# Kernel optimization log

Hardware: AMD Instinct MI355X
Metric: run time of the kernel (lower is better)

Reference implementation:

```python
import jax, jax.numpy as jnp
import numpy as np

N = 100000
E = 1600000
IN_C, HID_C, OUT_C = 128, 128, 10
NUM_GRAPHS = 64


def gcn_conv(x, src, dst, dinv, W, b, n_nodes):
    # x: [N, Fin]; src/dst: [E+N] (self-loops included); dinv: [N]
    xw = x @ W                                   # [N, Fout]
    norm = dinv[src] * dinv[dst]                 # [E+N]
    msg = xw[src] * norm[:, None]                # [E+N, Fout]
    return jax.ops.segment_sum(msg, dst, num_segments=n_nodes) + b


def setup_inputs() -> dict:
    key = jax.random.key(0)
    k1, k2, k3, k4, k5, k6, k7, k8 = jax.random.split(key, 8)
    x = jax.random.normal(k1, (N, IN_C), dtype=jnp.float32)
    edge_index = jax.random.randint(k2, (2, E), 0, N, dtype=jnp.int64)
    batch = jnp.sort(jax.random.randint(k3, (N,), 0, NUM_GRAPHS, dtype=jnp.int64))
    s1 = 1.0 / np.sqrt(IN_C)
    s2 = 1.0 / np.sqrt(HID_C)
    W1 = jax.random.uniform(k4, (IN_C, HID_C), jnp.float32, -s1, s1)
    b1 = jnp.zeros((HID_C,), jnp.float32)
    W2 = jax.random.uniform(k5, (HID_C, HID_C), jnp.float32, -s2, s2)
    b2 = jnp.zeros((HID_C,), jnp.float32)
    Wlin = jax.random.uniform(k6, (HID_C, OUT_C), jnp.float32, -s2, s2)
    blin = jax.random.uniform(k7, (OUT_C,), jnp.float32, -s2, s2)
    return {"x": x, "edge_index": edge_index, "batch": batch,
            "W1": W1, "b1": b1, "W2": W2, "b2": b2,
            "Wlin": Wlin, "blin": blin}


def reference(x, edge_index, batch, W1, b1, W2, b2, Wlin, blin):
    n = x.shape[0]
    loop = jnp.arange(n, dtype=edge_index.dtype)
    src = jnp.concatenate([edge_index[0], loop])   # self-loops appended
    dst = jnp.concatenate([edge_index[1], loop])
    deg = jax.ops.segment_sum(jnp.ones_like(dst, dtype=x.dtype), dst, num_segments=n)
    dinv = jnp.where(deg > 0, jax.lax.rsqrt(deg), 0.0)

    h = jax.nn.relu(gcn_conv(x, src, dst, dinv, W1, b1, n))
    h = jax.nn.relu(gcn_conv(h, src, dst, dinv, W2, b2, n))

    # global mean pool over graphs
    sums = jax.ops.segment_sum(h, batch, num_segments=NUM_GRAPHS)          # [G, H]
    cnts = jax.ops.segment_sum(jnp.ones((n,), h.dtype), batch, num_segments=NUM_GRAPHS)
    pooled = sums / jnp.maximum(cnts, 1.0)[:, None]
    return pooled @ Wlin + blin                                            # [G, OUT_C]
```

## Files before the change

### kernel.cpp

```cpp
#include <hip/hip_runtime.h>


#define TPB 256
#define R_LOG 7
#define R_NODES 128
#define NB_MAX 800
#define CH 8192
#define CAP_LOG 12
#define CAP 4096

#define FS 16.0f
#define FSI (1.0f / 16.0f)

typedef __attribute__((ext_vector_type(8))) short short8;
typedef __attribute__((ext_vector_type(4))) float f32x4;
typedef __attribute__((ext_vector_type(2))) float f32x2;

__device__ inline ushort f2bf(float x) {
    uint u = __float_as_uint(x);
    return (ushort)((u + 0x7FFFu + ((u >> 16) & 1u)) >> 16);
}

__global__ __launch_bounds__(1024) void bin_pass(const int* __restrict__ src,
                                                 const int* __restrict__ dst, int e,
                                                 int* __restrict__ gbcur,
                                                 int* __restrict__ buck, int nb) {
    __shared__ int vloc[CH];
    __shared__ ushort bidl[CH];
    __shared__ int cnts[NB_MAX], starts[NB_MAX], cnts2[NB_MAX];
    int t = threadIdx.x;
    for (int i = t; i < nb; i += 1024) { cnts[i] = 0; cnts2[i] = 0; }
    __syncthreads();
    int base = blockIdx.x * CH;
    int lim = base + CH; if (lim > e) lim = e;
    int ce = lim - base;
    int nv = ce >> 2;
    const int4* s4 = (const int4*)(src + base);
    const int4* d4 = (const int4*)(dst + base);
    for (int i = t; i < nv; i += 1024) {
        int4 s = s4[i], d = d4[i];
        int j = i << 2;
#define BIN1(J, SS, DD)                                                      \
        { int b_ = (DD) >> R_LOG;                                            \
          vloc[J] = ((SS) << R_LOG) | ((DD) & (R_NODES - 1));                \
          bidl[J] = (ushort)b_;                                              \
          atomicAdd(&cnts[b_], 1); }
        BIN1(j,     s.x, d.x)
        BIN1(j + 1, s.y, d.y)
        BIN1(j + 2, s.z, d.z)
        BIN1(j + 3, s.w, d.w)
    }
    for (int j = (nv << 2) + t; j < ce; j += 1024) {
        int dv = dst[base + j], sv = src[base + j];
        BIN1(j, sv, dv)
    }
#undef BIN1
    __syncthreads();
    for (int i = t; i < nb; i += 1024) {
        int c = cnts[i];
        starts[i] = c ? ((i << CAP_LOG) + atomicAdd(&gbcur[i], c)) : 0;
    }
    __syncthreads();
    for (int j = t; j < ce; j += 1024) {
        int b = bidl[j];
        int pos = starts[b] + atomicAdd(&cnts2[b], 1);
        if (pos < ((b + 1) << CAP_LOG))
            buck[pos] = vloc[j];
    }
}

__global__ __launch_bounds__(256) void count_pass(const int* __restrict__ buck,
                                                  const int* __restrict__ gbcur,
                                                  int* __restrict__ cnt,
                                                  float* __restrict__ dinv,
                                                  int* __restrict__ bktsum,
                                                  uint* __restrict__ t1z,
                                                  uint* __restrict__ t2z, int n) {
    __shared__ int c128[R_NODES];
    __shared__ int wred[4];
    int t = threadIdx.x;
    int b = blockIdx.x;
    if (b == 0 && t < 32) { t1z[t] = 0; t2z[t] = 0; }
    if (t < R_NODES) c128[t] = 0;
    __syncthreads();
    int beg = b << CAP_LOG;
    int fill = gbcur[b]; if (fill > CAP) fill = CAP;
    int end = beg + fill;
    int nv = fill >> 2;
    const int4* b4 = (const int4*)(buck + beg);
    for (int i = t; i < nv; i += 256) {
        int4 v = b4[i];
        atomicAdd(&c128[v.x & (R_NODES - 1)], 1);
        atomicAdd(&c128[v.y & (R_NODES - 1)], 1);
        atomicAdd(&c128[v.z & (R_NODES - 1)], 1);
        atomicAdd(&c128[v.w & (R_NODES - 1)], 1);
    }
    for (int i = beg + (nv << 2) + t; i < end; i += 256)
        atomicAdd(&c128[buck[i] & (R_NODES - 1)], 1);
    __syncthreads();
    int node = (b << R_LOG) + t;
    int pv = 0;
    if (t < R_NODES && node < n) {
        int c = c128[t];
        cnt[node] = c;
        dinv[node] = rsqrtf((float)(c + 1));
        pv = (c + 7) & ~7;
    }
    for (int o = 32; o; o >>= 1) pv += __shfl_down(pv, o);
    int lane = t & 63, wid = t >> 6;
    if (lane == 0) wred[wid] = pv;
    __syncthreads();
    if (t == 0) bktsum[b] = wred[0] + wred[1] + wred[2] + wred[3];
}

__device__ __forceinline__ void csr_body(int b, const int* __restrict__ buck,
                                         const int* __restrict__ cnt,
                                         const int* __restrict__ bktsum,
                                         const int* __restrict__ gbcur,
                                         int n, int nbkt, int* __restrict__ ew,
                                         int* __restrict__ rowptr) {
    __shared__ int rbase[R_NODES];
    __shared__ int cur[R_NODES];
    __shared__ int wtot[8], sred[8];
    int t = threadIdx.x;
    int n0 = b << R_LOG;
    int n1 = n0 + R_NODES; if (n1 > n) n1 = n;
    int nn = n1 - n0;
    int lane = t & 63, wid = t >> 6;
    int s = 0;
    for (int i = t; i < b; i += 512) s += bktsum[i];
    for (int o = 32; o; o >>= 1) s += __shfl_down(s, o);
    if (lane == 0) sred[wid] = s;
    int v = (t < nn) ? ((cnt[n0 + t] + 7) & ~7) : 0;
    int x = v;
    for (int o = 1; o < 64; o <<= 1) {
        int y = __shfl_up(x, o);
        if (lane >= o) x += y;
    }
    if (lane == 63) wtot[wid] = x;
    __syncthreads();
    int base = sred[0] + sred[1] + sred[2] + sred[3] +
               sred[4] + sred[5] + sred[6] + sred[7];
    int add = (wid == 1) ? wtot[0] : 0;
    int excl = base + x - v + add;
    if (t < nn) {
        rbase[t] = excl;
        rowptr[n0 + t] = excl;
        cur[t] = 0;
    }
    int endoff = base + wtot[0] + wtot[1];
    if (b == nbkt - 1 && t == 0) rowptr[n] = endoff;
    __syncthreads();
    int beg = b << CAP_LOG;
    int fill = gbcur[b]; if (fill > CAP) fill = CAP;
    int end = beg + fill;
    int nv = fill >> 2;
    const int4* bb4 = (const int4*)(buck + beg);
#define SCAT(VV) { int ld_ = (VV) & (R_NODES - 1);                       \
                   int p_ = rbase[ld_] + atomicAdd(&cur[ld_], 1);        \
                   ew[p_] = (VV) >> R_LOG; }
    for (int i = t; i < nv; i += 512) {
        int4 vv = bb4[i];
        SCAT(vv.x) SCAT(vv.y) SCAT(vv.z) SCAT(vv.w)
    }
    for (int i = beg + (nv << 2) + t; i < end; i += 512) {
        int vv = buck[i];
        SCAT(vv)
    }
#undef SCAT
    __syncthreads();
    if (t < nn) {
        int pe = (t + 1 < nn) ? rbase[t + 1] : endoff;
        for (int j = rbase[t] + cur[t]; j < pe; ++j) ew[j] = n;
    }
}

__device__ __forceinline__ void gemm1_body(int blk, const float* __restrict__ Av,
                                           const float* __restrict__ W,
                                           const float* __restrict__ dinv,
                                           uchar* __restrict__ C, int n) {
    __shared__ ushort Wt[128 * 136];
    int t = threadIdx.x;
    for (int idx = t; idx < 128 * 128; idx += 512) {
        int k = idx >> 7, nn = idx & 127;
        Wt[nn * 136 + k] = f2bf(W[idx]);
    }
    __syncthreads();

    int w = t >> 6, l = t & 63;
    int r0 = blk * 256;
    int lrow = l & 15, lhk = (l >> 4) * 8;

    short8 afrag[2][4];
    for (int mt = 0; mt < 2; ++mt) {
        int row = r0 + mt * 128 + w * 16 + lrow;
        bool ok = row < n;
        for (int ks = 0; ks < 4; ++ks) {
            int kb = ks * 32 + lhk;
            short8 f = {0, 0, 0, 0, 0, 0, 0, 0};
            if (ok) {
                const float* ap = Av + (size_t)row * 128 + kb;
                float4 u0 = *(const float4*)ap;
                float4 u1 = *(const float4*)(ap + 4);
                f[0] = (short)f2bf(u0.x); f[1] = (short)f2bf(u0.y);
                f[2] = (short)f2bf(u0.z); f[3] = (short)f2bf(u0.w);
                f[4] = (short)f2bf(u1.x); f[5] = (short)f2bf(u1.y);
                f[6] = (short)f2bf(u1.z); f[7] = (short)f2bf(u1.w);
            }
            afrag[mt][ks] = f;
        }
    }

    f32x4 acc[2][8];
    for (int mt = 0; mt < 2; ++mt)
        for (int nt = 0; nt < 8; ++nt)
            acc[mt][nt] = (f32x4){0.f, 0.f, 0.f, 0.f};

#pragma unroll
    for (int ks = 0; ks < 4; ++ks)
#pragma unroll
        for (int nt = 0; nt < 8; ++nt) {
            short8 b = *(const short8*)&Wt[(nt * 16 + lrow) * 136 + ks * 32 + lhk];
            acc[0][nt] = __builtin_amdgcn_mfma_f32_16x16x32_bf16(afrag[0][ks], b, acc[0][nt], 0, 0, 0);
            acc[1][nt] = __builtin_amdgcn_mfma_f32_16x16x32_bf16(afrag[1][ks], b, acc[1][nt], 0, 0, 0);
        }

    __syncthreads();
    uchar* Cs = (uchar*)Wt;
    int rb = (l >> 4) * 4;
    for (int mt = 0; mt < 2; ++mt)
        for (int r = 0; r < 4; ++r) {
            int lr = mt * 128 + w * 16 + rb + r;
            int rr = r0 + lr;
            float di = (rr < n) ? dinv[rr] * FS : 0.f;
            for (int nt = 0; nt < 8; ++nt) {
                float v = acc[mt][nt][r] * di;
                uint bb = (uint)__builtin_amdgcn_cvt_pk_fp8_f32(v, v, 0, false);
                Cs[lr * 128 + nt * 16 + lrow] = (uchar)(bb & 0xFF);
            }
        }
    __syncthreads();
    for (int idx = t; idx < 2048; idx += 512) {
        int rr = idx >> 3, cc = (idx & 7) * 16;
        int row2 = r0 + rr;
        if (row2 < n)
            *(uint4*)(C + (size_t)row2 * 128 + cc) = *(const uint4*)&Cs[rr * 128 + cc];
    }
}

__global__ __launch_bounds__(512) void csr_gemm1(const int* __restrict__ buck,
                                                 const int* __restrict__ cnt,
                                                 const int* __restrict__ bktsum,
                                                 const int* __restrict__ gbcur,
                                                 int n, int nbkt,
                                                 int* __restrict__ ew,
                                                 int* __restrict__ rowptr,
                                                 const float* __restrict__ x,
                                                 const float* __restrict__ W1,
                                                 const float* __restrict__ dinv,
                                                 uchar* __restrict__ T1) {
    int b = blockIdx.x;
    if (b < nbkt)
        csr_body(b, buck, cnt, bktsum, gbcur, n, nbkt, ew, rowptr);
    else
        gemm1_body(b - nbkt, x, W1, dinv, T1, n);
}

__global__ __launch_bounds__(512) void gemm2_pool(const ushort* __restrict__ A,
                                                  const float* __restrict__ W,
                                                  const float* __restrict__ bias,
                                                  const int* __restrict__ batch,
                                                  float* __restrict__ gsum,
                                                  float* __restrict__ gcnt, int n) {
    __shared__ ushort Wt[128 * 136];
    __shared__ float pg[2][128];
    __shared__ int bloc[256];
    __shared__ int cnt01[2];
    __shared__ int g01[2];
    int t = threadIdx.x;
    int r0 = blockIdx.x * 256;
    for (int idx = t; idx < 128 * 128; idx += 512) {
        int k = idx >> 7, nn = idx & 127;
        Wt[nn * 136 + k] = f2bf(W[idx]);
    }
    if (t < 256) {
        int row = r0 + t;
        bloc[t] = (row < n) ? batch[row] : -1;
    }
    if (t < 128) { pg[0][t] = 0.f; pg[1][t] = 0.f; }
    if (t < 2) cnt01[t] = 0;
    __syncthreads();
    if (t == 0) {
        g01[0] = bloc[0];
        int j = 255; while (j > 0 && bloc[j] < 0) --j;
        g01[1] = bloc[j];
    }

    int w = t >> 6, l = t & 63;
    int lrow = l & 15, lhk = (l >> 4) * 8;

    short8 afrag[2][4];
    for (int mt = 0; mt < 2; ++mt) {
        int row = r0 + mt * 128 + w * 16 + lrow;
        bool ok = row < n;
        for (int ks = 0; ks < 4; ++ks) {
            short8 f = {0, 0, 0, 0, 0, 0, 0, 0};
            if (ok) f = *(const short8*)(A + (size_t)row * 128 + ks * 32 + lhk);
            afrag[mt][ks] = f;
        }
    }

    f32x4 acc[2][8];
    for (int mt = 0; mt < 2; ++mt)
        for (int nt = 0; nt < 8; ++nt)
            acc[mt][nt] = (f32x4){0.f, 0.f, 0.f, 0.f};

#pragma unroll
    for (int ks = 0; ks < 4; ++ks)
#pragma unroll
        for (int nt = 0; nt < 8; ++nt) {
            short8 b = *(const short8*)&Wt[(nt * 16 + lrow) * 136 + ks * 32 + lhk];
            acc[0][nt] = __builtin_amdgcn_mfma_f32_16x16x32_bf16(afrag[0][ks], b, acc[0][nt], 0, 0, 0);
            acc[1][nt] = __builtin_amdgcn_mfma_f32_16x16x32_bf16(afrag[1][ks], b, acc[1][nt], 0, 0, 0);
        }
    __syncthreads();

    int g0 = g01[0], g1 = g01[1];
    float bch[8];
#pragma unroll
    for (int nt = 0; nt < 8; ++nt) bch[nt] = bias[nt * 16 + lrow];
    float ch0[8], ch1[8];
#pragma unroll
    for (int nt = 0; nt < 8; ++nt) { ch0[nt] = 0.f; ch1[nt] = 0.f; }
    int rb = (l >> 4) * 4;
    int c0 = 0, c1 = 0;
    for (int mt = 0; mt < 2; ++mt)
        for (int r = 0; r < 4; ++r) {
            int lr = mt * 128 + w * 16 + rb + r;
            int rr = r0 + lr;
            if (rr >= n) continue;
            int g = bloc[lr];
            if (g == g0) {
#pragma unroll
                for (int nt = 0; nt < 8; ++nt)
                    ch0[nt] += fmaxf(acc[mt][nt][r] + bch[nt], 0.f);
                if (lrow == 0) c0++;
            } else if (g == g1) {
#pragma unroll
                for (int nt = 0; nt < 8; ++nt)
                    ch1[nt] += fmaxf(acc[mt][nt][r] + bch[nt], 0.f);
                if (lrow == 0) c1++;
            } else {
#pragma unroll
                for (int nt = 0; nt < 8; ++nt)
                    atomicAdd(&gsum[g * 128 + nt * 16 + lrow],
                              fmaxf(acc[mt][nt][r] + bch[nt], 0.f));
                if (lrow == 0) atomicAdd(&gcnt[g], 1.f);
            }
        }
#pragma unroll
    for (int nt = 0; nt < 8; ++nt) {
        int ch = nt * 16 + lrow;
        atomicAdd(&pg[0][ch], ch0[nt]);
        atomicAdd(&pg[1][ch], ch1[nt]);
    }
    if (lrow == 0) {
        if (c0) atomicAdd(&cnt01[0], c0);
        if (c1) atomicAdd(&cnt01[1], c1);
    }
    __syncthreads();
    if (t < 128) {
        atomicAdd(&gsum[g0 * 128 + t], pg[0][t]);
        if (g1 != g0) atomicAdd(&gsum[g1 * 128 + t], pg[1][t]);
    }
    if (t == 0) {
        atomicAdd(&gcnt[g0], (float)cnt01[0]);
        if (g1 != g0) atomicAdd(&gcnt[g1], (float)cnt01[1]);
    }
}

#define LDG2(s) (*(const uint2*)(xwb + ((((uint)(s)) << 7) + clo)))
#define ACCU(G)                                                             \
    { f32x2 p01 = __builtin_amdgcn_cvt_pk_f32_fp8((int)(G).x, false);       \
      f32x2 p23 = __builtin_amdgcn_cvt_pk_f32_fp8((int)(G).x, true);        \
      f32x2 p45 = __builtin_amdgcn_cvt_pk_f32_fp8((int)(G).y, false);       \
      f32x2 p67 = __builtin_amdgcn_cvt_pk_f32_fp8((int)(G).y, true);        \
      a0 += p01.x; a1 += p01.y; a2 += p23.x; a3 += p23.y;                   \
      a4 += p45.x; a5 += p45.y; a6 += p67.x; a7 += p67.y; }

template <int MODE>
__global__ __launch_bounds__(256) void agg_gather(const uchar* __restrict__ tab,
                                                  const int* __restrict__ ewsrc,
                                                  const int* __restrict__ rowptr,
                                                  const float* __restrict__ dinv,
                                                  const float* __restrict__ bias,
                                                  void* __restrict__ outp, int n) {
    int node = blockIdx.x * 4 + (threadIdx.x >> 6);
    if (node >= n) return;
    int lane = threadIdx.x & 63;
    int q = lane >> 4;
    int cl = lane & 15;
    const char* xwb = (const char*)tab;
    uint clo = (uint)cl << 3;
    float a0 = 0.f, a1 = 0.f, a2 = 0.f, a3 = 0.f;
    float a4 = 0.f, a5 = 0.f, a6 = 0.f, a7 = 0.f;
    int beg = rowptr[node], end = rowptr[node + 1];
    int d8 = end - beg;

    if (d8 <= 32) {
        int sv = ewsrc[beg + (lane & 31)];
        int ng = d8 >> 3;
        uint2 A0, A1, B0, B1, C0, C1, D0, D1;
        if (ng > 0) { int s0 = __shfl(sv, q),      s1 = __shfl(sv, 4 + q);  A0 = LDG2(s0); A1 = LDG2(s1); }
        if (ng > 1) { int s0 = __shfl(sv, 8 + q),  s1 = __shfl(sv, 12 + q); B0 = LDG2(s0); B1 = LDG2(s1); }
        if (ng > 2) { int s0 = __shfl(sv, 16 + q), s1 = __shfl(sv, 20 + q); C0 = LDG2(s0); C1 = LDG2(s1); }
        if (ng > 3) { int s0 = __shfl(sv, 24 + q), s1 = __shfl(sv, 28 + q); D0 = LDG2(s0); D1 = LDG2(s1); }
        if (ng > 0) { ACCU(A0); ACCU(A1); }
        if (ng > 1) { ACCU(B0); ACCU(B1); }
        if (ng > 2) { ACCU(C0); ACCU(C1); }
        if (ng > 3) { ACCU(D0); ACCU(D1); }
    } else {
        for (int c = beg; c < end; c += 64) {
            int sv = ewsrc[c + lane];
            int ce = c + 64 < end ? c + 64 : end;
            int ngr = (ce - c) >> 3;
            int s0 = __shfl(sv, q), s1 = __shfl(sv, 4 + q);
            uint2 A0 = LDG2(s0), A1 = LDG2(s1);
            for (int g = 1; g < ngr; ++g) {
                int t0 = __shfl(sv, g * 8 + q), t1 = __shfl(sv, g * 8 + 4 + q);
                uint2 B0 = LDG2(t0), B1 = LDG2(t1);
                ACCU(A0); ACCU(A1);
                A0 = B0; A1 = B1;
            }
            ACCU(A0); ACCU(A1);
        }
    }

    a0 += __shfl_xor(a0, 16); a1 += __shfl_xor(a1, 16);
    a2 += __shfl_xor(a2, 16); a3 += __shfl_xor(a3, 16);
    a4 += __shfl_xor(a4, 16); a5 += __shfl_xor(a5, 16);
    a6 += __shfl_xor(a6, 16); a7 += __shfl_xor(a7, 16);
    a0 += __shfl_xor(a0, 32); a1 += __shfl_xor(a1, 32);
    a2 += __shfl_xor(a2, 32); a3 += __shfl_xor(a3, 32);
    a4 += __shfl_xor(a4, 32); a5 += __shfl_xor(a5, 32);
    a6 += __shfl_xor(a6, 32); a7 += __shfl_xor(a7, 32);
    if (lane < 16) {
        float di = dinv[node];
        float diS = di * FSI;
        uint2 sv2 = LDG2(node);
        f32x2 s01 = __builtin_amdgcn_cvt_pk_f32_fp8((int)sv2.x, false);
        f32x2 s23 = __builtin_amdgcn_cvt_pk_f32_fp8((int)sv2.x, true);
        f32x2 s45 = __builtin_amdgcn_cvt_pk_f32_fp8((int)sv2.y, false);
        f32x2 s67 = __builtin_amdgcn_cvt_pk_f32_fp8((int)sv2.y, true);
        if constexpr (MODE == 0) {
            const float4* b4 = (const float4*)bias;
            float4 bb0 = b4[cl * 2], bb1 = b4[cl * 2 + 1];
            float So = FS * di;
            float v0 = fmaxf(diS * (a0 + s01.x) + bb0.x, 0.f) * So;
            float v1 = fmaxf(diS * (a1 + s01.y) + bb0.y, 0.f) * So;
            float v2 = fmaxf(diS * (a2 + s23.x) + bb0.z, 0.f) * So;
            float v3 = fmaxf(diS * (a3 + s23.y) + bb0.w, 0.f) * So;
            float v4 = fmaxf(diS * (a4 + s45.x) + bb1.x, 0.f) * So;
            float v5 = fmaxf(diS * (a5 + s45.y) + bb1.y, 0.f) * So;
            float v6 = fmaxf(diS * (a6 + s67.x) + bb1.z, 0.f) * So;
            float v7 = fmaxf(diS * (a7 + s67.y) + bb1.w, 0.f) * So;
            uint lo = (uint)__builtin_amdgcn_cvt_pk_fp8_f32(v0, v1, 0, false);
            lo = (uint)__builtin_amdgcn_cvt_pk_fp8_f32(v2, v3, (int)lo, true);
            uint hi = (uint)__builtin_amdgcn_cvt_pk_fp8_f32(v4, v5, 0, false);
            hi = (uint)__builtin_amdgcn_cvt_pk_fp8_f32(v6, v7, (int)hi, true);
            uint2 r; r.x = lo; r.y = hi;
            *(uint2*)((char*)outp + ((size_t)node << 7) + clo) = r;
        } else {
            float v0 = diS * (a0 + s01.x);
            float v1 = diS * (a1 + s01.y);
            float v2 = diS * (a2 + s23.x);
            float v3 = diS * (a3 + s23.y);
            float v4 = diS * (a4 + s45.x);
            float v5 = diS * (a5 + s45.y);
            float v6 = diS * (a6 + s67.x);
            float v7 = diS * (a7 + s67.y);
            uint4 r;
            r.x = (uint)f2bf(v0) | ((uint)f2bf(v1) << 16);
            r.y = (uint)f2bf(v2) | ((uint)f2bf(v3) << 16);
            r.z = (uint)f2bf(v4) | ((uint)f2bf(v5) << 16);
            r.w = (uint)f2bf(v6) | ((uint)f2bf(v7) << 16);
            ((uint4*)outp)[(size_t)node * 16 + cl] = r;
        }
    }
}

__global__ __launch_bounds__(128) void final_kernel(const float* __restrict__ gsum,
                                                    const float* __restrict__ gcnt,
                                                    const float* __restrict__ Wlin,
                                                    const float* __restrict__ blin,
                                                    float* __restrict__ out) {
    __shared__ float pooled[128];
    int g = blockIdx.x;
    int c = threadIdx.x;
    float cntv = gcnt[g]; if (cntv < 1.f) cntv = 1.f;
    pooled[c] = gsum[g * 128 + c] / cntv;
    __syncthreads();
    if (c < 10) {
        float acc = blin[c];
        for (int k = 0; k < 128; ++k) acc += pooled[k] * Wlin[k * 10 + c];
        out[g * 10 + c] = acc;
    }
}

extern "C" void kernel_launch(void* const* d_in, const int* in_sizes, int n_in,
                              void* d_out, int out_size, void* d_ws, size_t ws_size,
                              hipStream_t stream) {
    const float* x    = (const float*)d_in[0];
    const int*   ei   = (const int*)d_in[1];
    const int*   batch= (const int*)d_in[2];
    const float* W1   = (const float*)d_in[3];
    const float* b1   = (const float*)d_in[4];
    const float* W2   = (const float*)d_in[5];
    const float* b2   = (const float*)d_in[6];
    const float* Wlin = (const float*)d_in[7];
    const float* blin = (const float*)d_in[8];
    float* out = (float*)d_out;

    const int n = in_sizes[0] / 128;
    const int e = in_sizes[1] / 2;
    const int* src = ei;
    const int* dst = ei + e;
    const int nb_bkt = (n + R_NODES - 1) >> R_LOG;

    char* ws = (char*)d_ws;
    size_t off = 0;
    auto take = [&](size_t bytes) -> char* {
        char* p = ws + off;
        off = (off + bytes + 255) & ~(size_t)255;
        return p;
    };
    int*    rowptr = (int*)   take((size_t)(n + 1) * 4);
    int*    cnt    = (int*)   take((size_t)n * 4);
    float*  dinv   = (float*) take((size_t)n * 4);
    int*    bktsum = (int*)   take((size_t)NB_MAX * 4);
    int*    ewsrc  = (int*)   take(((size_t)e + 7ull * (size_t)n + 64) * 4);
    uchar*  T1     = (uchar*) take((size_t)(n + 1) * 128);
    uchar*  T2     = (uchar*) take((size_t)(n + 1) * 128);
    ushort* V      = (ushort*)take((size_t)n * 128 * 2);
    int*    gbcur  = (int*)   take((size_t)NB_MAX * 4);
    float*  gsum   = (float*) take(64 * 128 * 4);
    float*  gcnt   = (float*) take(64 * 4);
    (void)ws_size;
    int* buck = (int*)V;

    size_t zspan = (size_t)((char*)gcnt + 64 * 4 - (char*)gbcur);
    hipMemsetAsync(gbcur, 0, zspan, stream);

    bin_pass<<<(e + CH - 1) / CH, 1024, 0, stream>>>(src, dst, e, gbcur, buck, nb_bkt);
    count_pass<<<nb_bkt, 256, 0, stream>>>(buck, gbcur, cnt, dinv, bktsum,
                                           (uint*)(T1 + (size_t)n * 128),
                                           (uint*)(T2 + (size_t)n * 128), n);

    const int gb256 = (n + 255) / 256;
    csr_gemm1<<<nb_bkt + gb256, 512, 0, stream>>>(buck, cnt, bktsum, gbcur, n, nb_bkt,
                                                  ewsrc, rowptr, x, W1, dinv, T1);

    agg_gather<0><<<(n + 3) / 4, 256, 0, stream>>>(T1, ewsrc, rowptr, dinv, b1, T2, n);
    agg_gather<1><<<(n + 3) / 4, 256, 0, stream>>>(T2, ewsrc, rowptr, dinv, b1, V, n);
    gemm2_pool<<<gb256, 512, 0, stream>>>(V, W2, b2, batch, gsum, gcnt, n);

    final_kernel<<<64, 128, 0, stream>>>(gsum, gcnt, Wlin, blin, out);
}
```

Measured before the change: 179.4 us.

## Process two GEMM tiles per block, reorder fused CSR/GEMM blocks, pack shuffles

Each GEMM1 and GEMM2 block now handles two 256-row tiles, so the bf16 transpose of the weight matrix into LDS is paid once per two tiles, and the block count is halved. GEMM1 gets a separate LDS staging buffer, writes half-tiles through it, and its blocks are placed before the CSR-build blocks in the fused launch. The gather kernel keeps its accumulators as float2 pairs and reduces them with 64-bit cross-lane shuffles, halving the shuffle count. The trade-offs are less parallelism per launch, a longer serial loop per block, and higher LDS use in the fused kernel.

```diff
diff --git a/kernel.cpp b/kernel.cpp
--- a/kernel.cpp
+++ b/kernel.cpp
@@ -19,6 +19,11 @@
 __device__ inline ushort f2bf(float x) {
     uint u = __float_as_uint(x);
     return (ushort)((u + 0x7FFFu + ((u >> 16) & 1u)) >> 16);
+}
+
+__device__ inline f32x2 shx2(f32x2 v, int m) {
+    double d = __shfl_xor(__builtin_bit_cast(double, v), m);
+    return __builtin_bit_cast(f32x2, d);
 }
 
 __global__ __launch_bounds__(1024) void bin_pass(const int* __restrict__ src,
@@ -175,11 +180,13 @@
     }
 }
 
-__device__ __forceinline__ void gemm1_body(int blk, const float* __restrict__ Av,
-                                           const float* __restrict__ W,
-                                           const float* __restrict__ dinv,
-                                           uchar* __restrict__ C, int n) {
+__device__ __forceinline__ void gemm1_persist(int bid, int ntiles,
+                                              const float* __restrict__ Av,
+                                              const float* __restrict__ W,
+                                              const float* __restrict__ dinv,
+                                              uchar* __restrict__ C, int n) {
     __shared__ ushort Wt[128 * 136];
+    __shared__ uchar Cs[128 * 128];
     int t = threadIdx.x;
     for (int idx = t; idx < 128 * 128; idx += 512) {
         int k = idx >> 7, nn = idx & 127;
@@ -188,63 +195,68 @@
     __syncthreads();
 
     int w = t >> 6, l = t & 63;
-    int r0 = blk * 256;
     int lrow = l & 15, lhk = (l >> 4) * 8;
-
-    short8 afrag[2][4];
-    for (int mt = 0; mt < 2; ++mt) {
-        int row = r0 + mt * 128 + w * 16 + lrow;
-        bool ok = row < n;
-        for (int ks = 0; ks < 4; ++ks) {
-            int kb = ks * 32 + lhk;
-            short8 f = {0, 0, 0, 0, 0, 0, 0, 0};
-            if (ok) {
-                const float* ap = Av + (size_t)row * 128 + kb;
-                float4 u0 = *(const float4*)ap;
-                float4 u1 = *(const float4*)(ap + 4);
-                f[0] = (short)f2bf(u0.x); f[1] = (short)f2bf(u0.y);
-                f[2] = (short)f2bf(u0.z); f[3] = (short)f2bf(u0.w);
-                f[4] = (short)f2bf(u1.x); f[5] = (short)f2bf(u1.y);
-                f[6] = (short)f2bf(u1.z); f[7] = (short)f2bf(u1.w);
-            }
-            afrag[mt][ks] = f;
-        }
-    }
-
-    f32x4 acc[2][8];
-    for (int mt = 0; mt < 2; ++mt)
-        for (int nt = 0; nt < 8; ++nt)
-            acc[mt][nt] = (f32x4){0.f, 0.f, 0.f, 0.f};
-
-#pragma unroll
-    for (int ks = 0; ks < 4; ++ks)
-#pragma unroll
-        for (int nt = 0; nt < 8; ++nt) {
-            short8 b = *(const short8*)&Wt[(nt * 16 + lrow) * 136 + ks * 32 + lhk];
-            acc[0][nt] = __builtin_amdgcn_mfma_f32_16x16x32_bf16(afrag[0][ks], b, acc[0][nt], 0, 0, 0);
-            acc[1][nt] = __builtin_amdgcn_mfma_f32_16x16x32_bf16(afrag[1][ks], b, acc[1][nt], 0, 0, 0);
-        }
-
-    __syncthreads();
-    uchar* Cs = (uchar*)Wt;
     int rb = (l >> 4) * 4;
-    for (int mt = 0; mt < 2; ++mt)
-        for (int r = 0; r < 4; ++r) {
-            int lr = mt * 128 + w * 16 + rb + r;
-            int rr = r0 + lr;
-            float di = (rr < n) ? dinv[rr] * FS : 0.f;
+
+    for (int ti = 0; ti < 2; ++ti) {
+        int tile = bid * 2 + ti;
+        if (tile >= ntiles) break;
+        int r0 = tile * 256;
+
+        short8 afrag[2][4];
+        for (int mt = 0; mt < 2; ++mt) {
+            int row = r0 + mt * 128 + w * 16 + lrow;
+            bool ok = row < n;
+            for (int ks = 0; ks < 4; ++ks) {
+                int kb = ks * 32 + lhk;
+                short8 f = {0, 0, 0, 0, 0, 0, 0, 0};
+                if (ok) {
+                    const float* ap = Av + (size_t)row * 128 + kb;
+                    float4 u0 = *(const float4*)ap;
+                    float4 u1 = *(const float4*)(ap + 4);
+                    f[0] = (short)f2bf(u0.x); f[1] = (short)f2bf(u0.y);
+                    f[2] = (short)f2bf(u0.z); f[3] = (short)f2bf(u0.w);
+                    f[4] = (short)f2bf(u1.x); f[5] = (short)f2bf(u1.y);
+                    f[6] = (short)f2bf(u1.z); f[7] = (short)f2bf(u1.w);
+                }
+                afrag[mt][ks] = f;
+            }
+        }
+
+        f32x4 acc[2][8];
+        for (int mt = 0; mt < 2; ++mt)
+            for (int nt = 0; nt < 8; ++nt)
+                acc[mt][nt] = (f32x4){0.f, 0.f, 0.f, 0.f};
+
+#pragma unroll
+        for (int ks = 0; ks < 4; ++ks)
+#pragma unroll
             for (int nt = 0; nt < 8; ++nt) {
-                float v = acc[mt][nt][r] * di;
-                uint bb = (uint)__builtin_amdgcn_cvt_pk_fp8_f32(v, v, 0, false);
-                Cs[lr * 128 + nt * 16 + lrow] = (uchar)(bb & 0xFF);
-            }
-        }
-    __syncthreads();
-    for (int idx = t; idx < 2048; idx += 512) {
-        int rr = idx >> 3, cc = (idx & 7) * 16;
-        int row2 = r0 + rr;
-        if (row2 < n)
-            *(uint4*)(C + (size_t)row2 * 128 + cc) = *(const uint4*)&Cs[rr * 128 + cc];
+                short8 b = *(const short8*)&Wt[(nt * 16 + lrow) * 136 + ks * 32 + lhk];
+                acc[0][nt] = __builtin_amdgcn_mfma_f32_16x16x32_bf16(afrag[0][ks], b, acc[0][nt], 0, 0, 0);
+                acc[1][nt] = __builtin_amdgcn_mfma_f32_16x16x32_bf16(afrag[1][ks], b, acc[1][nt], 0, 0, 0);
+            }
+
+        for (int mt = 0; mt < 2; ++mt) {
+            __syncthreads();
+            for (int r = 0; r < 4; ++r) {
+                int lrh = w * 16 + rb + r;
+                int rr = r0 + mt * 128 + lrh;
+                float di = (rr < n) ? dinv[rr] * FS : 0.f;
+                for (int nt = 0; nt < 8; ++nt) {
+                    float v = acc[mt][nt][r] * di;
+                    uint bb = (uint)__builtin_amdgcn_cvt_pk_fp8_f32(v, v, 0, false);
+                    Cs[lrh * 128 + nt * 16 + lrow] = (uchar)(bb & 0xFF);
+                }
+            }
+            __syncthreads();
+            for (int idx = t; idx < 1024; idx += 512) {
+                int rr = idx >> 3, cc = (idx & 7) * 16;
+                int row2 = r0 + mt * 128 + rr;
+                if (row2 < n)
+                    *(uint4*)(C + (size_t)row2 * 128 + cc) = *(const uint4*)&Cs[rr * 128 + cc];
+            }
+        }
     }
 }
 
@@ -252,7 +264,7 @@
                                                  const int* __restrict__ cnt,
                                                  const int* __restrict__ bktsum,
                                                  const int* __restrict__ gbcur,
-                                                 int n, int nbkt,
+                                                 int n, int nbkt, int ngem, int ntiles,
                                                  int* __restrict__ ew,
                                                  int* __restrict__ rowptr,
                                                  const float* __restrict__ x,
@@ -260,10 +272,10 @@
                                                  const float* __restrict__ dinv,
                                                  uchar* __restrict__ T1) {
     int b = blockIdx.x;
-    if (b < nbkt)
-        csr_body(b, buck, cnt, bktsum, gbcur, n, nbkt, ew, rowptr);
+    if (b < ngem)
+        gemm1_persist(b, ntiles, x, W1, dinv, T1, n);
     else
-        gemm1_body(b - nbkt, x, W1, dinv, T1, n);
+        csr_body(b - ngem, buck, cnt, bktsum, gbcur, n, nbkt, ew, rowptr);
 }
 
 __global__ __launch_bounds__(512) void gemm2_pool(const ushort* __restrict__ A,
@@ -271,122 +283,128 @@
                                                   const float* __restrict__ bias,
                                                   const int* __restrict__ batch,
                                                   float* __restrict__ gsum,
-                                                  float* __restrict__ gcnt, int n) {
+                                                  float* __restrict__ gcnt,
+                                                  int n, int ntiles) {
     __shared__ ushort Wt[128 * 136];
     __shared__ float pg[2][128];
     __shared__ int bloc[256];
     __shared__ int cnt01[2];
     __shared__ int g01[2];
     int t = threadIdx.x;
-    int r0 = blockIdx.x * 256;
     for (int idx = t; idx < 128 * 128; idx += 512) {
         int k = idx >> 7, nn = idx & 127;
         Wt[nn * 136 + k] = f2bf(W[idx]);
     }
-    if (t < 256) {
-        int row = r0 + t;
-        bloc[t] = (row < n) ? batch[row] : -1;
-    }
-    if (t < 128) { pg[0][t] = 0.f; pg[1][t] = 0.f; }
-    if (t < 2) cnt01[t] = 0;
-    __syncthreads();
-    if (t == 0) {
-        g01[0] = bloc[0];
-        int j = 255; while (j > 0 && bloc[j] < 0) --j;
-        g01[1] = bloc[j];
-    }
 
     int w = t >> 6, l = t & 63;
     int lrow = l & 15, lhk = (l >> 4) * 8;
-
-    short8 afrag[2][4];
-    for (int mt = 0; mt < 2; ++mt) {
-        int row = r0 + mt * 128 + w * 16 + lrow;
-        bool ok = row < n;
-        for (int ks = 0; ks < 4; ++ks) {
-            short8 f = {0, 0, 0, 0, 0, 0, 0, 0};
-            if (ok) f = *(const short8*)(A + (size_t)row * 128 + ks * 32 + lhk);
-            afrag[mt][ks] = f;
-        }
-    }
-
-    f32x4 acc[2][8];
-    for (int mt = 0; mt < 2; ++mt)
-        for (int nt = 0; nt < 8; ++nt)
-            acc[mt][nt] = (f32x4){0.f, 0.f, 0.f, 0.f};
-
-#pragma unroll
-    for (int ks = 0; ks < 4; ++ks)
+    int rb = (l >> 4) * 4;
+    float bch[8];
+#pragma unroll
+    for (int nt = 0; nt < 8; ++nt) bch[nt] = bias[nt * 16 + lrow];
+
+    for (int ti = 0; ti < 2; ++ti) {
+        int tile = blockIdx.x * 2 + ti;
+        if (tile >= ntiles) break;
+        int r0 = tile * 256;
+
+        __syncthreads();
+        if (t < 256) {
+            int row = r0 + t;
+            bloc[t] = (row < n) ? batch[row] : -1;
+        }
+        if (t < 128) { pg[0][t] = 0.f; pg[1][t] = 0.f; }
+        if (t < 2) cnt01[t] = 0;
+        __syncthreads();
+        if (t == 0) {
+            g01[0] = bloc[0];
+            int j = 255; while (j > 0 && bloc[j] < 0) --j;
+            g01[1] = bloc[j];
+        }
+
+        short8 afrag[2][4];
+        for (int mt = 0; mt < 2; ++mt) {
+            int row = r0 + mt * 128 + w * 16 + lrow;
+            bool ok = row < n;
+            for (int ks = 0; ks < 4; ++ks) {
+                short8 f = {0, 0, 0, 0, 0, 0, 0, 0};
+                if (ok) f = *(const short8*)(A + (size_t)row * 128 + ks * 32 + lhk);
+                afrag[mt][ks] = f;
+            }
+        }
+
+        f32x4 acc[2][8];
+        for (int mt = 0; mt < 2; ++mt)
+            for (int nt = 0; nt < 8; ++nt)
+                acc[mt][nt] = (f32x4){0.f, 0.f, 0.f, 0.f};
+
+#pragma unroll
+        for (int ks = 0; ks < 4; ++ks)
+#pragma unroll
+            for (int nt = 0; nt < 8; ++nt) {
+                short8 b = *(const short8*)&Wt[(nt * 16 + lrow) * 136 + ks * 32 + lhk];
+                acc[0][nt] = __builtin_amdgcn_mfma_f32_16x16x32_bf16(afrag[0][ks], b, acc[0][nt], 0, 0, 0);
+                acc[1][nt] = __builtin_amdgcn_mfma_f32_16x16x32_bf16(afrag[1][ks], b, acc[1][nt], 0, 0, 0);
+            }
+        __syncthreads();
+
+        int g0 = g01[0], g1 = g01[1];
+        float ch0[8], ch1[8];
+#pragma unroll
+        for (int nt = 0; nt < 8; ++nt) { ch0[nt] = 0.f; ch1[nt] = 0.f; }
+        int c0 = 0, c1 = 0;
+        for (int mt = 0; mt < 2; ++mt)
+            for (int r = 0; r < 4; ++r) {
+                int lr = mt * 128 + w * 16 + rb + r;
+                int rr = r0 + lr;
+                if (rr >= n) continue;
+                int g = bloc[lr];
+                if (g == g0) {
+#pragma unroll
+                    for (int nt = 0; nt < 8; ++nt)
+                        ch0[nt] += fmaxf(acc[mt][nt][r] + bch[nt], 0.f);
+                    if (lrow == 0) c0++;
+                } else if (g == g1) {
+#pragma unroll
+                    for (int nt = 0; nt < 8; ++nt)
+                        ch1[nt] += fmaxf(acc[mt][nt][r] + bch[nt], 0.f);
+                    if (lrow == 0) c1++;
+                } else {
+#pragma unroll
+                    for (int nt = 0; nt < 8; ++nt)
+                        atomicAdd(&gsum[g * 128 + nt * 16 + lrow],
+                                  fmaxf(acc[mt][nt][r] + bch[nt], 0.f));
+                    if (lrow == 0) atomicAdd(&gcnt[g], 1.f);
+                }
+            }
 #pragma unroll
         for (int nt = 0; nt < 8; ++nt) {
-            short8 b = *(const short8*)&Wt[(nt * 16 + lrow) * 136 + ks * 32 + lhk];
-            acc[0][nt] = __builtin_amdgcn_mfma_f32_16x16x32_bf16(afrag[0][ks], b, acc[0][nt], 0, 0, 0);
-            acc[1][nt] = __builtin_amdgcn_mfma_f32_16x16x32_bf16(afrag[1][ks], b, acc[1][nt], 0, 0, 0);
-        }
-    __syncthreads();
-
-    int g0 = g01[0], g1 = g01[1];
-    float bch[8];
-#pragma unroll
-    for (int nt = 0; nt < 8; ++nt) bch[nt] = bias[nt * 16 + lrow];
-    float ch0[8], ch1[8];
-#pragma unroll
-    for (int nt = 0; nt < 8; ++nt) { ch0[nt] = 0.f; ch1[nt] = 0.f; }
-    int rb = (l >> 4) * 4;
-    int c0 = 0, c1 = 0;
-    for (int mt = 0; mt < 2; ++mt)
-        for (int r = 0; r < 4; ++r) {
-            int lr = mt * 128 + w * 16 + rb + r;
-            int rr = r0 + lr;
-            if (rr >= n) continue;
-            int g = bloc[lr];
-            if (g == g0) {
-#pragma unroll
-                for (int nt = 0; nt < 8; ++nt)
-                    ch0[nt] += fmaxf(acc[mt][nt][r] + bch[nt], 0.f);
-                if (lrow == 0) c0++;
-            } else if (g == g1) {
-#pragma unroll
-                for (int nt = 0; nt < 8; ++nt)
-                    ch1[nt] += fmaxf(acc[mt][nt][r] + bch[nt], 0.f);
-                if (lrow == 0) c1++;
-            } else {
-#pragma unroll
-                for (int nt = 0; nt < 8; ++nt)
-                    atomicAdd(&gsum[g * 128 + nt * 16 + lrow],
-                              fmaxf(acc[mt][nt][r] + bch[nt], 0.f));
-                if (lrow == 0) atomicAdd(&gcnt[g], 1.f);
-            }
-        }
-#pragma unroll
-    for (int nt = 0; nt < 8; ++nt) {
-        int ch = nt * 16 + lrow;
-        atomicAdd(&pg[0][ch], ch0[nt]);
-        atomicAdd(&pg[1][ch], ch1[nt]);
-    }
-    if (lrow == 0) {
-        if (c0) atomicAdd(&cnt01[0], c0);
-        if (c1) atomicAdd(&cnt01[1], c1);
-    }
-    __syncthreads();
-    if (t < 128) {
-        atomicAdd(&gsum[g0 * 128 + t], pg[0][t]);
-        if (g1 != g0) atomicAdd(&gsum[g1 * 128 + t], pg[1][t]);
-    }
-    if (t == 0) {
-        atomicAdd(&gcnt[g0], (float)cnt01[0]);
-        if (g1 != g0) atomicAdd(&gcnt[g1], (float)cnt01[1]);
+            int ch = nt * 16 + lrow;
+            atomicAdd(&pg[0][ch], ch0[nt]);
+            atomicAdd(&pg[1][ch], ch1[nt]);
+        }
+        if (lrow == 0) {
+            if (c0) atomicAdd(&cnt01[0], c0);
+            if (c1) atomicAdd(&cnt01[1], c1);
+        }
+        __syncthreads();
+        if (t < 128) {
+            atomicAdd(&gsum[g0 * 128 + t], pg[0][t]);
+            if (g1 != g0) atomicAdd(&gsum[g1 * 128 + t], pg[1][t]);
+        }
+        if (t == 0) {
+            atomicAdd(&gcnt[g0], (float)cnt01[0]);
+            if (g1 != g0) atomicAdd(&gcnt[g1], (float)cnt01[1]);
+        }
     }
 }
 
 #define LDG2(s) (*(const uint2*)(xwb + ((((uint)(s)) << 7) + clo)))
 #define ACCU(G)                                                             \
-    { f32x2 p01 = __builtin_amdgcn_cvt_pk_f32_fp8((int)(G).x, false);       \
-      f32x2 p23 = __builtin_amdgcn_cvt_pk_f32_fp8((int)(G).x, true);        \
-      f32x2 p45 = __builtin_amdgcn_cvt_pk_f32_fp8((int)(G).y, false);       \
-      f32x2 p67 = __builtin_amdgcn_cvt_pk_f32_fp8((int)(G).y, true);        \
-      a0 += p01.x; a1 += p01.y; a2 += p23.x; a3 += p23.y;                   \
-      a4 += p45.x; a5 += p45.y; a6 += p67.x; a7 += p67.y; }
+    { a01 += __builtin_amdgcn_cvt_pk_f32_fp8((int)(G).x, false);            \
+      a23 += __builtin_amdgcn_cvt_pk_f32_fp8((int)(G).x, true);             \
+      a45 += __builtin_amdgcn_cvt_pk_f32_fp8((int)(G).y, false);            \
+      a67 += __builtin_amdgcn_cvt_pk_f32_fp8((int)(G).y, true); }
 
 template <int MODE>
 __global__ __launch_bounds__(256) void agg_gather(const uchar* __restrict__ tab,
@@ -402,8 +420,7 @@
     int cl = lane & 15;
     const char* xwb = (const char*)tab;
     uint clo = (uint)cl << 3;
-    float a0 = 0.f, a1 = 0.f, a2 = 0.f, a3 = 0.f;
-    float a4 = 0.f, a5 = 0.f, a6 = 0.f, a7 = 0.f;
+    f32x2 a01 = {0.f, 0.f}, a23 = {0.f, 0.f}, a45 = {0.f, 0.f}, a67 = {0.f, 0.f};
     int beg = rowptr[node], end = rowptr[node + 1];
     int d8 = end - beg;
 
@@ -436,14 +453,10 @@
         }
     }
 
-    a0 += __shfl_xor(a0, 16); a1 += __shfl_xor(a1, 16);
-    a2 += __shfl_xor(a2, 16); a3 += __shfl_xor(a3, 16);
-    a4 += __shfl_xor(a4, 16); a5 += __shfl_xor(a5, 16);
-    a6 += __shfl_xor(a6, 16); a7 += __shfl_xor(a7, 16);
-    a0 += __shfl_xor(a0, 32); a1 += __shfl_xor(a1, 32);
-    a2 += __shfl_xor(a2, 32); a3 += __shfl_xor(a3, 32);
-    a4 += __shfl_xor(a4, 32); a5 += __shfl_xor(a5, 32);
-    a6 += __shfl_xor(a6, 32); a7 += __shfl_xor(a7, 32);
+    a01 += shx2(a01, 16); a23 += shx2(a23, 16);
+    a45 += shx2(a45, 16); a67 += shx2(a67, 16);
+    a01 += shx2(a01, 32); a23 += shx2(a23, 32);
+    a45 += shx2(a45, 32); a67 += shx2(a67, 32);
     if (lane < 16) {
         float di = dinv[node];
         float diS = di * FSI;
@@ -456,14 +469,14 @@
             const float4* b4 = (const float4*)bias;
             float4 bb0 = b4[cl * 2], bb1 = b4[cl * 2 + 1];
             float So = FS * di;
-            float v0 = fmaxf(diS * (a0 + s01.x) + bb0.x, 0.f) * So;
-            float v1 = fmaxf(diS * (a1 + s01.y) + bb0.y, 0.f) * So;
-            float v2 = fmaxf(diS * (a2 + s23.x) + bb0.z, 0.f) * So;
-            float v3 = fmaxf(diS * (a3 + s23.y) + bb0.w, 0.f) * So;
-            float v4 = fmaxf(diS * (a4 + s45.x) + bb1.x, 0.f) * So;
-            float v5 = fmaxf(diS * (a5 + s45.y) + bb1.y, 0.f) * So;
-            float v6 = fmaxf(diS * (a6 + s67.x) + bb1.z, 0.f) * So;
-            float v7 = fmaxf(diS * (a7 + s67.y) + bb1.w, 0.f) * So;
+            float v0 = fmaxf(diS * (a01.x + s01.x) + bb0.x, 0.f) * So;
+            float v1 = fmaxf(diS * (a01.y + s01.y) + bb0.y, 0.f) * So;
+            float v2 = fmaxf(diS * (a23.x + s23.x) + bb0.z, 0.f) * So;
+            float v3 = fmaxf(diS * (a23.y + s23.y) + bb0.w, 0.f) * So;
+            float v4 = fmaxf(diS * (a45.x + s45.x) + bb1.x, 0.f) * So;
+            float v5 = fmaxf(diS * (a45.y + s45.y) + bb1.y, 0.f) * So;
+            float v6 = fmaxf(diS * (a67.x + s67.x) + bb1.z, 0.f) * So;
+            float v7 = fmaxf(diS * (a67.y + s67.y) + bb1.w, 0.f) * So;
             uint lo = (uint)__builtin_amdgcn_cvt_pk_fp8_f32(v0, v1, 0, false);
             lo = (uint)__builtin_amdgcn_cvt_pk_fp8_f32(v2, v3, (int)lo, true);
             uint hi = (uint)__builtin_amdgcn_cvt_pk_fp8_f32(v4, v5, 0, false);
@@ -471,14 +484,14 @@
             uint2 r; r.x = lo; r.y = hi;
             *(uint2*)((char*)outp + ((size_t)node << 7) + clo) = r;
         } else {
-            float v0 = diS * (a0 + s01.x);
-            float v1 = diS * (a1 + s01.y);
-            float v2 = diS * (a2 + s23.x);
-            float v3 = diS * (a3 + s23.y);
-            float v4 = diS * (a4 + s45.x);
-            float v5 = diS * (a5 + s45.y);
-            float v6 = diS * (a6 + s67.x);
-            float v7 = diS * (a7 + s67.y);
+            float v0 = diS * (a01.x + s01.x);
+            float v1 = diS * (a01.y + s01.y);
+            float v2 = diS * (a23.x + s23.x);
+            float v3 = diS * (a23.y + s23.y);
+            float v4 = diS * (a45.x + s45.x);
+            float v5 = diS * (a45.y + s45.y);
+            float v6 = diS * (a67.x + s67.x);
+            float v7 = diS * (a67.y + s67.y);
             uint4 r;
             r.x = (uint)f2bf(v0) | ((uint)f2bf(v1) << 16);
             r.y = (uint)f2bf(v2) | ((uint)f2bf(v3) << 16);
@@ -556,13 +569,15 @@
                                            (uint*)(T1 + (size_t)n * 128),
                                            (uint*)(T2 + (size_t)n * 128), n);
 
-    const int gb256 = (n + 255) / 256;
-    csr_gemm1<<<nb_bkt + gb256, 512, 0, stream>>>(buck, cnt, bktsum, gbcur, n, nb_bkt,
-                                                  ewsrc, rowptr, x, W1, dinv, T1);
+    const int ntiles = (n + 255) / 256;
+    const int ngem = (ntiles + 1) / 2;
+    csr_gemm1<<<ngem + nb_bkt, 512, 0, stream>>>(buck, cnt, bktsum, gbcur, n, nb_bkt,
+                                                 ngem, ntiles, ewsrc, rowptr,
+                                                 x, W1, dinv, T1);
 
     agg_gather<0><<<(n + 3) / 4, 256, 0, stream>>>(T1, ewsrc, rowptr, dinv, b1, T2, n);
     agg_gather<1><<<(n + 3) / 4, 256, 0, stream>>>(T2, ewsrc, rowptr, dinv, b1, V, n);
-    gemm2_pool<<<gb256, 512, 0, stream>>>(V, W2, b2, batch, gsum, gcnt, n);
+    gemm2_pool<<<ngem, 512, 0, stream>>>(V, W2, b2, batch, gsum, gcnt, n, ntiles);
 
     final_kernel<<<64, 128, 0, stream>>>(gsum, gcnt, Wlin, blin, out);
 }
```

Result: no change. 178.9 us (-0.3%).
